# Optimization experiments

Hardware: AMD Instinct MI355X
Metric: run time of the kernel (lower is better)

## Reference

```python
import jax, jax.numpy as jnp
import numpy as np

N_NODES, N_EDGES, N_GRAPHS, N_FEATS = 100000, 1600000, 256, 128
BN_EPS = 1e-5


def setup_inputs() -> dict:
    key = jax.random.key(0)
    ks = jax.random.split(key, 12)
    x = jax.random.normal(ks[0], (N_NODES, N_FEATS), jnp.float32)
    edge_index = jax.random.randint(ks[1], (2, N_EDGES), 0, N_NODES, dtype=jnp.int64)
    batch = jnp.sort(jax.random.randint(ks[2], (N_NODES,), 0, N_GRAPHS, dtype=jnp.int64))
    s = 0.05
    return {
        "x": x,
        "edge_index": edge_index,
        "batch": batch,
        "W1": jax.random.normal(ks[3], (N_FEATS, 32), jnp.float32) * s,
        "b1": jnp.zeros((32,), jnp.float32),
        "W2": jax.random.normal(ks[4], (32, 64), jnp.float32) * s,
        "b2": jnp.zeros((64,), jnp.float32),
        "fcW1": jax.random.normal(ks[5], (64, 32), jnp.float32) * s,
        "fcb1": jnp.zeros((32,), jnp.float32),
        "gamma": jnp.ones((32,), jnp.float32),
        "beta": jnp.zeros((32,), jnp.float32),
        "fcW2": jax.random.normal(ks[6], (32, 1), jnp.float32) * s,
        "fcb2": jnp.zeros((1,), jnp.float32),
    }


def _gcn_conv(x, src, dst, deg_inv, W, b):
    # PyG GCNConv: h = x @ W; out[d] = sum_e norm_e * h[src_e] + self-loop + b
    h = x @ W  # [N, out]
    norm = deg_inv[src] * deg_inv[dst]  # [E]
    msg = h[src] * norm[:, None]
    out = jax.ops.segment_sum(msg, dst, num_segments=x.shape[0])
    out = out + (deg_inv * deg_inv)[:, None] * h  # self-loop contribution
    return out + b


def reference(x, edge_index, batch, W1, b1, W2, b2, fcW1, fcb1, gamma, beta, fcW2, fcb2):
    src, dst = edge_index[0], edge_index[1]
    n = x.shape[0]
    # degree with self loops, computed on target nodes (PyG default)
    deg = 1.0 + jax.ops.segment_sum(jnp.ones_like(src, dtype=x.dtype), dst, num_segments=n)
    deg_inv = jax.lax.rsqrt(deg)
    h = _gcn_conv(x, src, dst, deg_inv, W1, b1)   # [N, 32]
    h = _gcn_conv(h, src, dst, deg_inv, W2, b2)   # [N, 64]
    # scatter_mean over graph batch
    sums = jax.ops.segment_sum(h, batch, num_segments=N_GRAPHS)  # [G, 64]
    cnt = jax.ops.segment_sum(jnp.ones((n,), h.dtype), batch, num_segments=N_GRAPHS)
    pooled = sums / jnp.maximum(cnt, 1.0)[:, None]
    # head: Linear -> ReLU -> BatchNorm1d (batch stats) -> Dropout(eval=id) -> Linear -> Softplus
    z = jax.nn.relu(pooled @ fcW1 + fcb1)  # [G, 32]
    mu = jnp.mean(z, axis=0)
    var = jnp.var(z, axis=0)
    z = (z - mu) * jax.lax.rsqrt(var + BN_EPS) * gamma + beta
    out = jax.nn.softplus(z @ fcW2 + fcb2)  # [G, 1]
    return out
```

## Files before the change

kernel.cpp:

```cpp
#include <hip/hip_runtime.h>

#define NN 100000
#define NE 1600000
#define NG 256

#define BSH 8
#define NPB 256
#define NBKT ((NN + NPB - 1) / NPB)
#define STRIDE 4608
#define TILE 8192
#define NB_P1 ((NE + TILE - 1) / TILE)

__device__ __forceinline__ unsigned short f2bf(float x) {
    unsigned int u = __float_as_uint(x);
    u += 0x7FFFu + ((u >> 16) & 1u);
    return (unsigned short)(u >> 16);
}
__device__ __forceinline__ float2 bf2x2(unsigned int v) {
    float2 r;
    r.x = __uint_as_float(v << 16);
    r.y = __uint_as_float(v & 0xFFFF0000u);
    return r;
}
__device__ __forceinline__ unsigned int bfpack(float x, float y) {
    return (unsigned int)f2bf(x) | ((unsigned int)f2bf(y) << 16);
}

__global__ __launch_bounds__(1024) void part_kernel(const int* __restrict__ src,
                                                    const int* __restrict__ dst,
                                                    int* __restrict__ bkt_cur,
                                                    int* __restrict__ epack) {
    __shared__ int hist[512];
    __shared__ int scan0[512];
    __shared__ int cur[NBKT];
    __shared__ int gbase[NBKT];
    __shared__ int stage[TILE];
    __shared__ unsigned short sb[TILE];
    int tid = threadIdx.x;
    int e0 = blockIdx.x * TILE;
    int e1 = min(e0 + TILE, NE);
    int n = e1 - e0;

    for (int i = tid; i < 512; i += 1024) hist[i] = 0;
    __syncthreads();

    int d_[8], s_[8];
#pragma unroll
    for (int k = 0; k < 8; ++k) {
        int e = e0 + tid + k * 1024;
        if (e < e1) {
            d_[k] = dst[e];
            s_[k] = src[e];
            atomicAdd(&hist[d_[k] >> BSH], 1);
        }
    }
    __syncthreads();

    if (tid < 512) scan0[tid] = hist[tid];
    __syncthreads();
    for (int off = 1; off < 512; off <<= 1) {
        int t = (tid < 512 && tid >= off) ? scan0[tid - off] : 0;
        __syncthreads();
        if (tid < 512) scan0[tid] += t;
        __syncthreads();
    }
    if (tid < NBKT) {
        int h = hist[tid];
        int ex = scan0[tid] - h;
        cur[tid] = ex;
        gbase[tid] = tid * STRIDE + (h ? atomicAdd(&bkt_cur[tid], h) : 0) - ex;
    }
    __syncthreads();

#pragma unroll
    for (int k = 0; k < 8; ++k) {
        int e = e0 + tid + k * 1024;
        if (e < e1) {
            int d = d_[k];
            int bk = d >> BSH;
            int p = atomicAdd(&cur[bk], 1);
            stage[p] = s_[k] | ((d & (NPB - 1)) << 17);
            sb[p] = (unsigned short)bk;
        }
    }
    __syncthreads();

    for (int j = tid; j < n; j += 1024) {
        int bk = sb[j];
        int a = gbase[bk] + j;
        if (a < (bk + 1) * STRIDE)
            epack[a] = stage[j];
    }
}

__global__ __launch_bounds__(512) void build_kernel(const int* __restrict__ epack,
                                                    const int* __restrict__ bkt_cur,
                                                    int* __restrict__ row_beg,
                                                    int* __restrict__ row_deg,
                                                    int* __restrict__ col,
                                                    float* __restrict__ deg_inv) {
    __shared__ int cnt[NPB];
    __shared__ int ts[NPB];
    int b = blockIdx.x;
    int tid = threadIdx.x;
    int ebase = b * STRIDE;
    int eend = ebase + min(bkt_cur[b], STRIDE);
    int nbase = b << BSH;
    if (tid < NPB) cnt[tid] = 0;
    __syncthreads();
    for (int e = ebase + tid; e < eend; e += 512)
        atomicAdd(&cnt[epack[e] >> 17], 1);
    __syncthreads();
    int v = 0;
    if (tid < NPB) {
        v = cnt[tid];
        ts[tid] = v;
    }
    __syncthreads();
    for (int off = 1; off < NPB; off <<= 1) {
        int t = (tid < NPB && tid >= off) ? ts[tid - off] : 0;
        __syncthreads();
        if (tid < NPB) ts[tid] += t;
        __syncthreads();
    }
    if (tid < NPB) {
        int loff = ts[tid] - v;
        int node = nbase + tid;
        if (node < NN) {
            row_beg[node] = ebase + loff;
            row_deg[node] = v;
            deg_inv[node] = rsqrtf(1.0f + (float)v);
        }
        cnt[tid] = loff;
    }
    __syncthreads();
    for (int e = ebase + tid; e < eend; e += 512) {
        int rec = epack[e];
        int r = atomicAdd(&cnt[rec >> 17], 1);
        col[ebase + r] = rec & 0x1FFFF;
    }
}

__global__ __launch_bounds__(256) void gemm_x_w1(const float* __restrict__ x,
                                                 const float* __restrict__ W,
                                                 const float* __restrict__ deg_inv,
                                                 unsigned short* __restrict__ h, int N) {
    __shared__ float wsh[128 * 32];
    __shared__ float xs[32][132];
    int tid = threadIdx.x;
    int row0 = blockIdx.x * 32;
    if (blockIdx.x == 0 && tid < 8)
        *(ushort4*)&h[(size_t)NN * 32 + tid * 4] = make_ushort4(0, 0, 0, 0);
    for (int i = tid; i < 1024; i += 256)
        ((float4*)wsh)[i] = ((const float4*)W)[i];
    for (int i = tid; i < 1024; i += 256) {
        int r = i >> 5, c4 = i & 31;
        *(float4*)&xs[r][c4 * 4] = ((const float4*)(x + (size_t)(row0 + r) * 128))[c4];
    }
    __syncthreads();
    int r = tid >> 3;
    int c8 = (tid & 7) * 4;
    float acc0 = 0.f, acc1 = 0.f, acc2 = 0.f, acc3 = 0.f;
#pragma unroll
    for (int k0 = 0; k0 < 128; k0 += 4) {
        float4 xv = *(const float4*)&xs[r][k0];
#pragma unroll
        for (int j = 0; j < 4; ++j) {
            float xk = (&xv.x)[j];
            float4 wv = *(const float4*)&wsh[(k0 + j) * 32 + c8];
            acc0 += xk * wv.x;
            acc1 += xk * wv.y;
            acc2 += xk * wv.z;
            acc3 += xk * wv.w;
        }
    }
    float di = deg_inv[row0 + r];
    ushort4 o;
    o.x = f2bf(acc0 * di);
    o.y = f2bf(acc1 * di);
    o.z = f2bf(acc2 * di);
    o.w = f2bf(acc3 * di);
    *(ushort4*)&h[(size_t)(row0 + r) * 32 + c8] = o;
}

template <int MODE>
__global__ __launch_bounds__(512) void conv_bf_kernel(const int* __restrict__ row_beg,
                                                      const int* __restrict__ row_deg,
                                                      const int* __restrict__ col,
                                                      const uint2* __restrict__ h2,
                                                      const float* __restrict__ deg_inv,
                                                      const float* __restrict__ b,
                                                      uint2* __restrict__ out_bf,
                                                      const int* __restrict__ batch,
                                                      float* __restrict__ gsum,
                                                      float* __restrict__ gcnt) {
    __shared__ float sacc[2][32];
    __shared__ float scnt[2];
    __shared__ int sg[2];
    int tid = threadIdx.x;
    int gid = blockIdx.x * 512 + tid;
    int node = gid >> 3;
    int L = gid & 7;
    if (MODE == 0) {
        if (blockIdx.x == 0 && tid < 8)
            out_bf[(size_t)NN * 8 + tid] = make_uint2(0u, 0u);
    } else {
        if (tid < 64) sacc[tid >> 5][tid & 31] = 0.f;
        if (tid < 2) scnt[tid] = 0.f;
        if (tid == 0) {
            int nb = blockIdx.x * 64;
            sg[0] = batch[nb];
            sg[1] = batch[min(nb + 63, NN - 1)];
        }
    }
    bool valid = node < NN;
    float o0 = 0.f, o1 = 0.f, o2 = 0.f, o3 = 0.f;
    if (valid) {
        int beg = row_beg[node];
        int end = beg + row_deg[node];
        uint2 sv = h2[node * 8 + L];
        float2 s0 = bf2x2(sv.x), s1 = bf2x2(sv.y);
        float a00 = s0.x, a01 = s0.y, a02 = s1.x, a03 = s1.y;
        float a10 = 0.f, a11 = 0.f, a12 = 0.f, a13 = 0.f;
        float a20 = 0.f, a21 = 0.f, a22 = 0.f, a23 = 0.f;
        float a30 = 0.f, a31 = 0.f, a32 = 0.f, a33 = 0.f;
        int myc = (beg + L < end) ? col[beg + L] : NN;
        for (int j0 = beg; j0 < end; j0 += 8) {
            int nxt = (j0 + 8 + L < end) ? col[j0 + 8 + L] : NN;
            int i0 = __shfl(myc, 0, 8) * 8 + L;
            int i1 = __shfl(myc, 1, 8) * 8 + L;
            int i2 = __shfl(myc, 2, 8) * 8 + L;
            int i3 = __shfl(myc, 3, 8) * 8 + L;
            int i4 = __shfl(myc, 4, 8) * 8 + L;
            int i5 = __shfl(myc, 5, 8) * 8 + L;
            int i6 = __shfl(myc, 6, 8) * 8 + L;
            int i7 = __shfl(myc, 7, 8) * 8 + L;
            uint2 v0 = h2[i0];
            uint2 v1 = h2[i1];
            uint2 v2 = h2[i2];
            uint2 v3 = h2[i3];
            uint2 v4 = h2[i4];
            uint2 v5 = h2[i5];
            uint2 v6 = h2[i6];
            uint2 v7 = h2[i7];
            float2 p, q;
            p = bf2x2(v0.x); q = bf2x2(v0.y);
            a00 += p.x; a01 += p.y; a02 += q.x; a03 += q.y;
            p = bf2x2(v1.x); q = bf2x2(v1.y);
            a10 += p.x; a11 += p.y; a12 += q.x; a13 += q.y;
            p = bf2x2(v2.x); q = bf2x2(v2.y);
            a20 += p.x; a21 += p.y; a22 += q.x; a23 += q.y;
            p = bf2x2(v3.x); q = bf2x2(v3.y);
            a30 += p.x; a31 += p.y; a32 += q.x; a33 += q.y;
            p = bf2x2(v4.x); q = bf2x2(v4.y);
            a00 += p.x; a01 += p.y; a02 += q.x; a03 += q.y;
            p = bf2x2(v5.x); q = bf2x2(v5.y);
            a10 += p.x; a11 += p.y; a12 += q.x; a13 += q.y;
            p = bf2x2(v6.x); q = bf2x2(v6.y);
            a20 += p.x; a21 += p.y; a22 += q.x; a23 += q.y;
            p = bf2x2(v7.x); q = bf2x2(v7.y);
            a30 += p.x; a31 += p.y; a32 += q.x; a33 += q.y;
            myc = nxt;
        }
        float c0 = (a00 + a10) + (a20 + a30);
        float c1 = (a01 + a11) + (a21 + a31);
        float c2 = (a02 + a12) + (a22 + a32);
        float c3 = (a03 + a13) + (a23 + a33);
        float di = deg_inv[node];
        if (MODE == 0) {
            o0 = di * di * c0 + di * b[4 * L + 0];
            o1 = di * di * c1 + di * b[4 * L + 1];
            o2 = di * di * c2 + di * b[4 * L + 2];
            o3 = di * di * c3 + di * b[4 * L + 3];
            out_bf[node * 8 + L] = make_uint2(bfpack(o0, o1), bfpack(o2, o3));
        } else {
            o0 = di * c0; o1 = di * c1; o2 = di * c2; o3 = di * c3;
        }
    }
    if (MODE == 1) {
        __syncthreads();
        if (valid) {
            int gn = batch[node];
            int fb = 4 * L;
            if (gn == sg[0]) {
                atomicAdd(&sacc[0][fb + 0], o0);
                atomicAdd(&sacc[0][fb + 1], o1);
                atomicAdd(&sacc[0][fb + 2], o2);
                atomicAdd(&sacc[0][fb + 3], o3);
                if (L == 0) atomicAdd(&scnt[0], 1.f);
            } else if (gn == sg[1]) {
                atomicAdd(&sacc[1][fb + 0], o0);
                atomicAdd(&sacc[1][fb + 1], o1);
                atomicAdd(&sacc[1][fb + 2], o2);
                atomicAdd(&sacc[1][fb + 3], o3);
                if (L == 0) atomicAdd(&scnt[1], 1.f);
            } else {
                unsafeAtomicAdd(&gsum[gn * 32 + fb + 0], o0);
                unsafeAtomicAdd(&gsum[gn * 32 + fb + 1], o1);
                unsafeAtomicAdd(&gsum[gn * 32 + fb + 2], o2);
                unsafeAtomicAdd(&gsum[gn * 32 + fb + 3], o3);
                if (L == 0) unsafeAtomicAdd(&gcnt[gn], 1.f);
            }
        }
        __syncthreads();
        if (tid < 64) {
            int s = tid >> 5, f = tid & 31;
            if (s == 0 || sg[1] != sg[0])
                unsafeAtomicAdd(&gsum[sg[s] * 32 + f], sacc[s][f]);
        }
        if (tid == 0) unsafeAtomicAdd(&gcnt[sg[0]], scnt[0]);
        if (tid == 1 && sg[1] != sg[0]) unsafeAtomicAdd(&gcnt[sg[1]], scnt[1]);
    }
}

__global__ __launch_bounds__(256) void head_kernel(const float* __restrict__ gsum,
                                                   const float* __restrict__ gcnt,
                                                   const float* __restrict__ W2,
                                                   const float* __restrict__ b2,
                                                   const float* __restrict__ fcW1,
                                                   const float* __restrict__ fcb1,
                                                   const float* __restrict__ gamma,
                                                   const float* __restrict__ beta,
                                                   const float* __restrict__ fcW2,
                                                   const float* __restrict__ fcb2,
                                                   float* __restrict__ out) {
    __shared__ float zs[NG][33];
    __shared__ float wcs[32 * 32];
    __shared__ float bcs[32];
    __shared__ float part1[8][32];
    __shared__ float part2[8][32];
    __shared__ float mu[32], rstd[32];
    int g = threadIdx.x;

    for (int idx = g; idx < 32 * 32; idx += 256) {
        int k = idx / 32, ch = idx % 32;
        float a = 0.f;
#pragma unroll
        for (int j = 0; j < 64; ++j) a += W2[k * 64 + j] * fcW1[j * 32 + ch];
        wcs[idx] = a;
    }
    if (g < 32) {
        float a = fcb1[g];
#pragma unroll
        for (int j = 0; j < 64; ++j) a += b2[j] * fcW1[j * 32 + g];
        bcs[g] = a;
    }
    __syncthreads();

    float p32[32];
    float inv = 1.0f / fmaxf(gcnt[g], 1.0f);
    {
        const float4* gs4 = (const float4*)(gsum + g * 32);
#pragma unroll
        for (int q = 0; q < 8; ++q) {
            float4 v = gs4[q];
            p32[q * 4 + 0] = v.x * inv;
            p32[q * 4 + 1] = v.y * inv;
            p32[q * 4 + 2] = v.z * inv;
            p32[q * 4 + 3] = v.w * inv;
        }
    }
#pragma unroll 4
    for (int ch = 0; ch < 32; ++ch) {
        float acc = bcs[ch];
#pragma unroll
        for (int k = 0; k < 32; ++k) acc += p32[k] * wcs[k * 32 + ch];
        zs[g][ch] = fmaxf(acc, 0.f);
    }
    __syncthreads();

    {
        int ch = g & 31, seg = g >> 5;
        float s = 0.f, sq = 0.f;
#pragma unroll
        for (int i = 0; i < 32; ++i) {
            float v = zs[seg * 32 + i][ch];
            s += v;
            sq += v * v;
        }
        part1[seg][ch] = s;
        part2[seg][ch] = sq;
    }
    __syncthreads();
    if (g < 32) {
        float s = 0.f, sq = 0.f;
#pragma unroll
        for (int i = 0; i < 8; ++i) { s += part1[i][g]; sq += part2[i][g]; }
        float m = s / NG;
        float v = sq / NG - m * m;
        mu[g] = m;
        rstd[g] = rsqrtf(fmaxf(v, 0.f) + 1e-5f);
    }
    __syncthreads();

    float acc = fcb2[0];
#pragma unroll 4
    for (int ch = 0; ch < 32; ++ch) {
        float zn = (zs[g][ch] - mu[ch]) * rstd[ch] * gamma[ch] + beta[ch];
        acc += zn * fcW2[ch];
    }
    out[g] = fmaxf(acc, 0.f) + log1pf(expf(-fabsf(acc)));
}

extern "C" void kernel_launch(void* const* d_in, const int* in_sizes, int n_in,
                              void* d_out, int out_size, void* d_ws, size_t ws_size,
                              hipStream_t stream) {
    const float* x     = (const float*)d_in[0];
    const int*   ei    = (const int*)d_in[1];
    const int*   batch = (const int*)d_in[2];
    const float* W1    = (const float*)d_in[3];
    const float* b1    = (const float*)d_in[4];
    const float* W2    = (const float*)d_in[5];
    const float* b2    = (const float*)d_in[6];
    const float* fcW1  = (const float*)d_in[7];
    const float* fcb1  = (const float*)d_in[8];
    const float* gamma = (const float*)d_in[9];
    const float* beta  = (const float*)d_in[10];
    const float* fcW2  = (const float*)d_in[11];
    const float* fcb2  = (const float*)d_in[12];
    float* out = (float*)d_out;

    char* p = (char*)d_ws;
    int*   bkt_cur = (int*)p;        p += 400 * 4;
    float* gsum    = (float*)p;      p += (size_t)NG * 32 * 4;
    float* gcnt    = (float*)p;      p += (size_t)NG * 4;
    float* deg_inv = (float*)p;      p += (size_t)NN * 4;
    int*   row_beg = (int*)p;        p += (size_t)(NN + 8) * 4;
    int*   row_deg = (int*)p;        p += (size_t)(NN + 8) * 4;
    int*   epack   = (int*)p;        p += (size_t)NBKT * STRIDE * 4;
    int*   col     = (int*)p;        p += (size_t)NBKT * STRIDE * 4;
    unsigned short* h1s = (unsigned short*)p;  p += (size_t)(NN + 1) * 32 * 2;
    uint2*          t1  = (uint2*)p;           p += (size_t)(NN + 1) * 8 * 8;

    const int* srcv = ei;
    const int* dstv = ei + NE;

    hipMemsetAsync(bkt_cur, 0, 400 * 4 + (size_t)NG * 32 * 4 + (size_t)NG * 4, stream);

    part_kernel<<<NB_P1, 1024, 0, stream>>>(srcv, dstv, bkt_cur, epack);
    build_kernel<<<NBKT, 512, 0, stream>>>(epack, bkt_cur, row_beg, row_deg, col, deg_inv);

    gemm_x_w1<<<NN / 32, 256, 0, stream>>>(x, W1, deg_inv, h1s, NN);
    conv_bf_kernel<0><<<((size_t)NN * 8 + 511) / 512, 512, 0, stream>>>(
        row_beg, row_deg, col, (const uint2*)h1s, deg_inv, b1, t1, nullptr, nullptr, nullptr);

    conv_bf_kernel<1><<<((size_t)NN * 8 + 511) / 512, 512, 0, stream>>>(
        row_beg, row_deg, col, (const uint2*)t1, deg_inv, b1, nullptr, batch, gsum, gcnt);

    head_kernel<<<1, 256, 0, stream>>>(gsum, gcnt, W2, b2, fcW1, fcb1, gamma, beta, fcW2, fcb2, out);
}
```

Measured before the change: 218.8 us.

## Use nontemporal loads for streamed inputs and widen head kernel to 1024 threads

Streaming reads of edge indices, x rows and CSR column indices now use nontemporal loads, which is meant to keep the L2 free for the gathered feature rows. The x loads are split into four scalar nontemporal loads where there was one float4 load, so each load instruction moves less data. The single-block head kernel grows from 256 to 1024 threads: four threads share each graph's 32 output channels, and the folded weight product is computed one entry per thread. This shortens the serial latency of the tail kernel but adds more reduction partials.

```diff
diff --git a/kernel.cpp b/kernel.cpp
--- a/kernel.cpp
+++ b/kernel.cpp
@@ -49,8 +49,8 @@
     for (int k = 0; k < 8; ++k) {
         int e = e0 + tid + k * 1024;
         if (e < e1) {
-            d_[k] = dst[e];
-            s_[k] = src[e];
+            d_[k] = __builtin_nontemporal_load(&dst[e]);
+            s_[k] = __builtin_nontemporal_load(&src[e]);
             atomicAdd(&hist[d_[k] >> BSH], 1);
         }
     }
@@ -155,7 +155,13 @@
         ((float4*)wsh)[i] = ((const float4*)W)[i];
     for (int i = tid; i < 1024; i += 256) {
         int r = i >> 5, c4 = i & 31;
-        *(float4*)&xs[r][c4 * 4] = ((const float4*)(x + (size_t)(row0 + r) * 128))[c4];
+        const float* xp = x + (size_t)(row0 + r) * 128 + c4 * 4;
+        float v0 = __builtin_nontemporal_load(xp + 0);
+        float v1 = __builtin_nontemporal_load(xp + 1);
+        float v2 = __builtin_nontemporal_load(xp + 2);
+        float v3 = __builtin_nontemporal_load(xp + 3);
+        float* dp = &xs[r][c4 * 4];
+        dp[0] = v0; dp[1] = v1; dp[2] = v2; dp[3] = v3;
     }
     __syncthreads();
     int r = tid >> 3;
@@ -224,9 +230,9 @@
         float a10 = 0.f, a11 = 0.f, a12 = 0.f, a13 = 0.f;
         float a20 = 0.f, a21 = 0.f, a22 = 0.f, a23 = 0.f;
         float a30 = 0.f, a31 = 0.f, a32 = 0.f, a33 = 0.f;
-        int myc = (beg + L < end) ? col[beg + L] : NN;
+        int myc = (beg + L < end) ? __builtin_nontemporal_load(&col[beg + L]) : NN;
         for (int j0 = beg; j0 < end; j0 += 8) {
-            int nxt = (j0 + 8 + L < end) ? col[j0 + 8 + L] : NN;
+            int nxt = (j0 + 8 + L < end) ? __builtin_nontemporal_load(&col[j0 + 8 + L]) : NN;
             int i0 = __shfl(myc, 0, 8) * 8 + L;
             int i1 = __shfl(myc, 1, 8) * 8 + L;
             int i2 = __shfl(myc, 2, 8) * 8 + L;
@@ -313,31 +319,38 @@
     }
 }
 
-__global__ __launch_bounds__(256) void head_kernel(const float* __restrict__ gsum,
-                                                   const float* __restrict__ gcnt,
-                                                   const float* __restrict__ W2,
-                                                   const float* __restrict__ b2,
-                                                   const float* __restrict__ fcW1,
-                                                   const float* __restrict__ fcb1,
-                                                   const float* __restrict__ gamma,
-                                                   const float* __restrict__ beta,
-                                                   const float* __restrict__ fcW2,
-                                                   const float* __restrict__ fcb2,
-                                                   float* __restrict__ out) {
+__global__ __launch_bounds__(1024) void head_kernel(const float* __restrict__ gsum,
+                                                    const float* __restrict__ gcnt,
+                                                    const float* __restrict__ W2,
+                                                    const float* __restrict__ b2,
+                                                    const float* __restrict__ fcW1,
+                                                    const float* __restrict__ fcb1,
+                                                    const float* __restrict__ gamma,
+                                                    const float* __restrict__ beta,
+                                                    const float* __restrict__ fcW2,
+                                                    const float* __restrict__ fcb2,
+                                                    float* __restrict__ out) {
     __shared__ float zs[NG][33];
     __shared__ float wcs[32 * 32];
     __shared__ float bcs[32];
-    __shared__ float part1[8][32];
-    __shared__ float part2[8][32];
+    __shared__ float part1[32][32];
+    __shared__ float part2[32][32];
     __shared__ float mu[32], rstd[32];
     int g = threadIdx.x;
 
-    for (int idx = g; idx < 32 * 32; idx += 256) {
-        int k = idx / 32, ch = idx % 32;
+    {
+        int k = g >> 5, ch = g & 31;
+        const float4* w2r = (const float4*)(W2 + k * 64);
         float a = 0.f;
 #pragma unroll
-        for (int j = 0; j < 64; ++j) a += W2[k * 64 + j] * fcW1[j * 32 + ch];
-        wcs[idx] = a;
+        for (int j4 = 0; j4 < 16; ++j4) {
+            float4 w = w2r[j4];
+            a += w.x * fcW1[(j4 * 4 + 0) * 32 + ch];
+            a += w.y * fcW1[(j4 * 4 + 1) * 32 + ch];
+            a += w.z * fcW1[(j4 * 4 + 2) * 32 + ch];
+            a += w.w * fcW1[(j4 * 4 + 3) * 32 + ch];
+        }
+        wcs[g] = a;
     }
     if (g < 32) {
         float a = fcb1[g];
@@ -347,10 +360,11 @@
     }
     __syncthreads();
 
-    float p32[32];
-    float inv = 1.0f / fmaxf(gcnt[g], 1.0f);
     {
-        const float4* gs4 = (const float4*)(gsum + g * 32);
+        int gr = g >> 2, sub = g & 3;
+        float inv = 1.0f / fmaxf(gcnt[gr], 1.0f);
+        float p32[32];
+        const float4* gs4 = (const float4*)(gsum + gr * 32);
 #pragma unroll
         for (int q = 0; q < 8; ++q) {
             float4 v = gs4[q];
@@ -359,13 +373,14 @@
             p32[q * 4 + 2] = v.z * inv;
             p32[q * 4 + 3] = v.w * inv;
         }
-    }
-#pragma unroll 4
-    for (int ch = 0; ch < 32; ++ch) {
-        float acc = bcs[ch];
-#pragma unroll
-        for (int k = 0; k < 32; ++k) acc += p32[k] * wcs[k * 32 + ch];
-        zs[g][ch] = fmaxf(acc, 0.f);
+#pragma unroll
+        for (int cc = 0; cc < 8; ++cc) {
+            int ch = sub * 8 + cc;
+            float acc = bcs[ch];
+#pragma unroll
+            for (int k = 0; k < 32; ++k) acc += p32[k] * wcs[k * 32 + ch];
+            zs[gr][ch] = fmaxf(acc, 0.f);
+        }
     }
     __syncthreads();
 
@@ -373,8 +388,8 @@
         int ch = g & 31, seg = g >> 5;
         float s = 0.f, sq = 0.f;
 #pragma unroll
-        for (int i = 0; i < 32; ++i) {
-            float v = zs[seg * 32 + i][ch];
+        for (int i = 0; i < 8; ++i) {
+            float v = zs[seg * 8 + i][ch];
             s += v;
             sq += v * v;
         }
@@ -385,7 +400,7 @@
     if (g < 32) {
         float s = 0.f, sq = 0.f;
 #pragma unroll
-        for (int i = 0; i < 8; ++i) { s += part1[i][g]; sq += part2[i][g]; }
+        for (int i = 0; i < 32; ++i) { s += part1[i][g]; sq += part2[i][g]; }
         float m = s / NG;
         float v = sq / NG - m * m;
         mu[g] = m;
@@ -393,13 +408,15 @@
     }
     __syncthreads();
 
-    float acc = fcb2[0];
+    if (g < NG) {
+        float acc = fcb2[0];
 #pragma unroll 4
-    for (int ch = 0; ch < 32; ++ch) {
-        float zn = (zs[g][ch] - mu[ch]) * rstd[ch] * gamma[ch] + beta[ch];
-        acc += zn * fcW2[ch];
-    }
-    out[g] = fmaxf(acc, 0.f) + log1pf(expf(-fabsf(acc)));
+        for (int ch = 0; ch < 32; ++ch) {
+            float zn = (zs[g][ch] - mu[ch]) * rstd[ch] * gamma[ch] + beta[ch];
+            acc += zn * fcW2[ch];
+        }
+        out[g] = fmaxf(acc, 0.f) + log1pf(expf(-fabsf(acc)));
+    }
 }
 
 extern "C" void kernel_launch(void* const* d_in, const int* in_sizes, int n_in,
@@ -435,7 +452,7 @@
     const int* srcv = ei;
     const int* dstv = ei + NE;
 
-    hipMemsetAsync(bkt_cur, 0, 400 * 4 + (size_t)NG * 32 * 4 + (size_t)NG * 4, stream);
+    (void)hipMemsetAsync(bkt_cur, 0, 400 * 4 + (size_t)NG * 32 * 4 + (size_t)NG * 4, stream);
 
     part_kernel<<<NB_P1, 1024, 0, stream>>>(srcv, dstv, bkt_cur, epack);
     build_kernel<<<NBKT, 512, 0, stream>>>(epack, bkt_cur, row_beg, row_deg, col, deg_inv);
@@ -447,5 +464,5 @@
     conv_bf_kernel<1><<<((size_t)NN * 8 + 511) / 512, 512, 0, stream>>>(
         row_beg, row_deg, col, (const uint2*)t1, deg_inv, b1, nullptr, batch, gsum, gcnt);
 
-    head_kernel<<<1, 256, 0, stream>>>(gsum, gcnt, W2, b2, fcW1, fcb1, gamma, beta, fcW2, fcb2, out);
-}
+    head_kernel<<<1, 1024, 0, stream>>>(gsum, gcnt, W2, b2, fcW1, fcb1, gamma, beta, fcW2, fcb2, out);
+}
```

After: 226.9 us. 3.7% more time.
